# Optimization experiments

Measured on AMD Instinct MI355X. Metric: run time of the kernel, lower is better.

## Reference

```python
import jax, jax.numpy as jnp
import numpy as np
from jax import lax


def setup_inputs() -> dict:
    key = jax.random.key(0)
    ks = jax.random.split(key, 3)
    N, Cin, Cout, H, W = 4, 256, 256, 96, 96
    x = jax.random.normal(ks[0], (N, Cin, H, W), jnp.float32)
    # DCNv2-style internal offset/mask conv: 27 = 9 dy + 9 dx + 9 mask logits
    w_off = jax.random.normal(ks[1], (27, Cin, 3, 3), jnp.float32) * 0.01
    b_off = jnp.zeros((27,), jnp.float32)
    w = jax.random.normal(ks[2], (Cout, Cin, 3, 3), jnp.float32) * (1.0 / np.sqrt(Cin * 9))
    b = jnp.zeros((Cout,), jnp.float32)
    gamma = jnp.ones((Cout,), jnp.float32)
    beta = jnp.zeros((Cout,), jnp.float32)
    return {"x": x, "w_off": w_off, "b_off": b_off, "w": w, "b": b, "gamma": gamma, "beta": beta}


def _bilinear(img, py, px):
    # img: [C,H,W]; py,px: [K,H,W] float sampling coords. Zero outside bounds.
    C, H, W = img.shape
    flat = img.reshape(C, -1)
    y0 = jnp.floor(py)
    x0 = jnp.floor(px)
    ly = py - y0
    lx = px - x0

    def gather(yc, xc):
        valid = (yc >= 0) & (yc <= H - 1) & (xc >= 0) & (xc <= W - 1)
        yi = jnp.clip(yc, 0, H - 1).astype(jnp.int32)
        xi = jnp.clip(xc, 0, W - 1).astype(jnp.int32)
        idx = (yi * W + xi).reshape(-1)
        v = flat[:, idx].reshape((C,) + yc.shape)  # [C,K,H,W]
        return v * valid.astype(img.dtype)

    v00 = gather(y0, x0)
    v01 = gather(y0, x0 + 1)
    v10 = gather(y0 + 1, x0)
    v11 = gather(y0 + 1, x0 + 1)
    return (v00 * (1 - ly) * (1 - lx) + v01 * (1 - ly) * lx
            + v10 * ly * (1 - lx) + v11 * ly * lx)


def _forward(x, w_off, b_off, w, b, gamma, beta):
    N, C, H, W = x.shape
    Cout = w.shape[0]
    dn = ("NCHW", "OIHW", "NCHW")
    # internal offset/mask conv (3x3, stride 1, pad 1)
    om = lax.conv_general_dilated(x, w_off, (1, 1), [(1, 1), (1, 1)], dimension_numbers=dn)
    om = om + b_off[None, :, None, None]
    dy, dx, m = om[:, :9], om[:, 9:18], jax.nn.sigmoid(om[:, 18:])
    # base 3x3 kernel grid, dilation 1, padding 1 (centered taps -1..1)
    ky, kx = jnp.meshgrid(jnp.arange(3) - 1, jnp.arange(3) - 1, indexing="ij")
    py = dy + jnp.arange(H, dtype=x.dtype)[None, None, :, None] + ky.reshape(1, 9, 1, 1).astype(x.dtype)
    px = dx + jnp.arange(W, dtype=x.dtype)[None, None, None, :] + kx.reshape(1, 9, 1, 1).astype(x.dtype)
    sampled = jax.vmap(_bilinear)(x, py, px)  # [N,C,9,H,W]
    sampled = sampled * m[:, None]            # DCNv2 modulation mask
    y = jnp.einsum("nckhw,ock->nohw", sampled, w.reshape(Cout, C, 9))
    y = y + b[None, :, None, None]
    # BatchNorm2d (training-mode batch statistics) + ReLU
    mean = y.mean(axis=(0, 2, 3))
    var = y.var(axis=(0, 2, 3))
    y = (y - mean[None, :, None, None]) * lax.rsqrt(var[None, :, None, None] + 1e-5)
    y = y * gamma[None, :, None, None] + beta[None, :, None, None]
    return jax.nn.relu(y)


def reference(x, w_off, b_off, w, b, gamma, beta):
    return _forward(x, w_off, b_off, w, b, gamma, beta)
```

## Files before the change

### kernel.cpp

```cpp
#include <hip/hip_runtime.h>
#include <cmath>

#define H 96
#define W 96
#define HW 9216
#define CIN 256
#define COUT 256
#define NB 4
#define NCH 72
#define NGR 36

typedef float f32x4 __attribute__((ext_vector_type(4)));
typedef float f32x2 __attribute__((ext_vector_type(2)));
typedef short bf16x8 __attribute__((ext_vector_type(8)));

__device__ __forceinline__ unsigned short f2bf(float f) {
  unsigned int u = __float_as_uint(f);
  u += 0x7fff + ((u >> 16) & 1);
  return (unsigned short)(u >> 16);
}
__device__ __forceinline__ float bf2f(unsigned short u) {
  return __uint_as_float(((unsigned int)u) << 16);
}
__device__ __forceinline__ f32x2 up2(unsigned int u) {
  f32x2 r;
  r.x = __uint_as_float(u << 16);
  r.y = __uint_as_float(u & 0xffff0000u);
  return r;
}
__device__ __forceinline__ unsigned int cvtpk(float lo, float hi) {
  unsigned int r;
  asm("v_cvt_pk_bf16_f32 %0, %1, %2" : "=v"(r) : "v"(lo), "v"(hi));
  return r;
}

__device__ __forceinline__ void bar() {
  asm volatile("s_waitcnt lgkmcnt(0)" ::: "memory");
  __builtin_amdgcn_s_barrier();
  asm volatile("" ::: "memory");
}

__global__ __launch_bounds__(256)
void xt_convert(const float* __restrict__ x, unsigned short* __restrict__ xT) {
  __shared__ unsigned short ls[64][72];
  int tid = threadIdx.x;
  int hwbase = blockIdx.x * 64;
  int cbase  = blockIdx.y * 64;
  int n      = blockIdx.z;

  {
    int cl = tid >> 2, qd = tid & 3;
    const float* src = x + ((size_t)(n * CIN + cbase + cl)) * HW + hwbase + qd * 16;
#pragma unroll
    for (int m = 0; m < 4; ++m) {
      float4 v = *(const float4*)(src + m * 4);
      int hwl = qd * 16 + m * 4;
      ls[hwl + 0][cl] = f2bf(v.x);
      ls[hwl + 1][cl] = f2bf(v.y);
      ls[hwl + 2][cl] = f2bf(v.z);
      ls[hwl + 3][cl] = f2bf(v.w);
    }
  }
  __syncthreads();
  {
    int hw = tid >> 2, part = tid & 3;
    unsigned short* dst = xT + ((size_t)(n * HW + hwbase + hw)) * CIN + cbase + part * 16;
    *(uint4*)(dst + 0) = *(const uint4*)(&ls[hw][part * 16 + 0]);
    *(uint4*)(dst + 8) = *(const uint4*)(&ls[hw][part * 16 + 8]);
  }
}

__global__ __launch_bounds__(256)
void wa_convert(const float* __restrict__ w, unsigned short* __restrict__ Ag) {
  int gid = blockIdx.x * 256 + threadIdx.x;
  int ch = gid >> 10;
  int rest = gid & 1023;
  int ot = rest >> 6, l = rest & 63;
  int o = ot * 16 + (l & 15);
  int k = ch >> 3, cc = ch & 7;
  int cbase = cc * 32 + (l >> 4) * 8;
  unsigned short r[8];
#pragma unroll
  for (int j = 0; j < 8; ++j)
    r[j] = f2bf(w[((size_t)o * CIN + cbase + j) * 9 + k]);
  uint4 pk;
  pk.x = (unsigned int)r[0] | ((unsigned int)r[1] << 16);
  pk.y = (unsigned int)r[2] | ((unsigned int)r[3] << 16);
  pk.z = (unsigned int)r[4] | ((unsigned int)r[5] << 16);
  pk.w = (unsigned int)r[6] | ((unsigned int)r[7] << 16);
  *(uint4*)(Ag + (size_t)gid * 8) = pk;
}

__global__ __launch_bounds__(256)
void wa2_convert(const float* __restrict__ w_off, unsigned short* __restrict__ Ag2) {
  int gid = blockIdx.x * 256 + threadIdx.x;
  int ch = gid >> 7;
  int rest = gid & 127;
  int ot = rest >> 6, l = rest & 63;
  int o = ot * 16 + (l & 15);
  int k = ch >> 3, cc = ch & 7;
  int cbase = cc * 32 + (l >> 4) * 8;
  unsigned short r[8];
#pragma unroll
  for (int j = 0; j < 8; ++j)
    r[j] = (o < 27) ? f2bf(w_off[((size_t)o * CIN + cbase + j) * 9 + k]) : (unsigned short)0;
  uint4 pk;
  pk.x = (unsigned int)r[0] | ((unsigned int)r[1] << 16);
  pk.y = (unsigned int)r[2] | ((unsigned int)r[3] << 16);
  pk.z = (unsigned int)r[4] | ((unsigned int)r[5] << 16);
  pk.w = (unsigned int)r[6] | ((unsigned int)r[7] << 16);
  *(uint4*)(Ag2 + (size_t)gid * 8) = pk;
}

__global__ __launch_bounds__(256, 4)
void offset_gemm(const unsigned short* __restrict__ xT,
                 const unsigned short* __restrict__ Ag2,
                 const float* __restrict__ b_off,
                 float* __restrict__ py, float* __restrict__ px,
                 float* __restrict__ mk) {
  __shared__ int sPos[9][64];
  __shared__ unsigned short sB[2][4096];

  int tid = threadIdx.x;
  int wv = tid >> 6, lane = tid & 63, quad = lane >> 4, l16 = lane & 15;
  int pixBase = blockIdx.x * 64;
  int n = blockIdx.y;
  const unsigned short* xTn = xT + (size_t)n * HW * CIN;

  if (tid < 64) {
    int hwp = pixBase + tid;
    int hh = hwp / W, wx = hwp % W;
#pragma unroll
    for (int ty = 0; ty < 3; ++ty) {
#pragma unroll
      for (int tx = 0; tx < 3; ++tx) {
        int iy = hh + ty - 1, ix = wx + tx - 1;
        bool ok = (iy >= 0) && (iy < H) && (ix >= 0) && (ix < W);
        sPos[ty * 3 + tx][tid] = ok ? (iy * W + ix) : -1;
      }
    }
  }
  bar();

  int pix0 = tid >> 3, ck0 = tid & 7;
  int pix1 = 32 + (tid >> 3);
  int a0 = (ck0 >> 2) * 2048 + (pix0 >> 4) * 512 + ((ck0 & 3) * 16 + ((pix0 & 15) ^ (ck0 & 3))) * 8;
  int a1 = (ck0 >> 2) * 2048 + (pix1 >> 4) * 512 + ((ck0 & 3) * 16 + ((pix1 & 15) ^ (ck0 & 3))) * 8;

  f32x4 acc[2];
  acc[0] = (f32x4){0.f, 0.f, 0.f, 0.f};
  acc[1] = (f32x4){0.f, 0.f, 0.f, 0.f};

  uint4 dA[2], dB[2];
  auto issue = [&](int g, uint4* d) {
    int k = g % 9, c2 = g / 9;
    int p0 = sPos[k][pix0], p1 = sPos[k][pix1];
    d[0] = (uint4){0, 0, 0, 0};
    d[1] = (uint4){0, 0, 0, 0};
    if (p0 >= 0) d[0] = *(const uint4*)(xTn + (size_t)p0 * CIN + c2 * 64 + ck0 * 8);
    if (p1 >= 0) d[1] = *(const uint4*)(xTn + (size_t)p1 * CIN + c2 * 64 + ck0 * 8);
  };

  bf16x8 afr[4];
  auto aload = [&](int g) {
    int k = g % 9, c2 = g / 9;
    int ch = k * 8 + c2 * 2;
#pragma unroll
    for (int s = 0; s < 2; ++s)
#pragma unroll
      for (int ot = 0; ot < 2; ++ot)
        afr[s * 2 + ot] = *(const bf16x8*)(Ag2 + ((size_t)((ch + s) * 2 + ot) * 64 + lane) * 8);
  };

  int rdAddr0 = wv * 512 + (quad * 16 + (l16 ^ quad)) * 8;
  auto mfmaPhase = [&](int buf) {
    __builtin_amdgcn_s_setprio(1);
#pragma unroll
    for (int s = 0; s < 2; ++s) {
      bf16x8 bfr = *(const bf16x8*)(&sB[buf][s * 2048 + rdAddr0]);
      acc[0] = __builtin_amdgcn_mfma_f32_16x16x32_bf16(afr[s * 2 + 0], bfr, acc[0], 0, 0, 0);
      acc[1] = __builtin_amdgcn_mfma_f32_16x16x32_bf16(afr[s * 2 + 1], bfr, acc[1], 0, 0, 0);
    }
    __builtin_amdgcn_s_setprio(0);
  };
  auto store = [&](uint4* d, int buf) {
    *(uint4*)(&sB[buf][a0]) = d[0];
    *(uint4*)(&sB[buf][a1]) = d[1];
  };

  issue(0, dA);
  aload(0);
  store(dA, 0);
  issue(1, dB);
  bar();

  for (int g = 0; g < NGR; g += 2) {
    if (g + 2 < NGR) issue(g + 2, dA);
    mfmaPhase(0);
    aload(g + 1);
    store(dB, 1);
    bar();

    if (g + 3 < NGR) issue(g + 3, dB);
    mfmaPhase(1);
    if (g + 2 < NGR) {
      aload(g + 2);
      store(dA, 0);
      bar();
    }
  }

  int pix = pixBase + wv * 16 + l16;
  int he = pix / W, we = pix % W;
#pragma unroll
  for (int ot = 0; ot < 2; ++ot) {
#pragma unroll
    for (int r = 0; r < 4; ++r) {
      int kk = ot * 16 + quad * 4 + r;
      if (kk >= 27) continue;
      float v = acc[ot][r] + b_off[kk];
      if (kk < 9) {
        py[(size_t)(n * 9 + kk) * HW + pix] = v + (float)he + (float)(kk / 3 - 1);
      } else if (kk < 18) {
        int j = kk - 9;
        px[(size_t)(n * 9 + j) * HW + pix] = v + (float)we + (float)(j % 3 - 1);
      } else {
        mk[(size_t)(n * 9 + (kk - 18)) * HW + pix] = 1.f / (1.f + expf(-v));
      }
    }
  }
}

__global__ __launch_bounds__(512, 4)
void fused_gemm(const unsigned short* __restrict__ xT,
                const unsigned short* __restrict__ Ag,
                const float* __restrict__ py,
                const float* __restrict__ px,
                const float* __restrict__ mk,
                unsigned short* __restrict__ yb,
                float* __restrict__ sumArr, float* __restrict__ sqArr) {
  __shared__ int   sIdx[9][4][64];
  __shared__ float sWgt[9][4][64];
  __shared__ unsigned short sB[2][4096];

  int tid = threadIdx.x;
  int wv = tid >> 6, lane = tid & 63, quad = lane >> 4, l16 = lane & 15;
  int pixBase = blockIdx.x * 64;
  int n = blockIdx.y;
  const unsigned short* xTn = xT + (size_t)n * HW * CIN;

  {
    int pix0 = tid & 63;
    int k0 = tid >> 6;
#pragma unroll
    for (int rep = 0; rep < 2; ++rep) {
      int k = (rep == 0) ? k0 : 8;
      if (rep == 1 && tid >= 64) break;
      int off = (n * 9 + k) * HW + pixBase + pix0;
      float fy = py[off], fx = px[off], fm = mk[off];
      float y0f = floorf(fy), x0f = floorf(fx);
      float ly = fy - y0f, lx = fx - x0f;
      int y0 = (int)y0f, x0 = (int)x0f;
      int cy0 = min(max(y0, 0), H - 1), cy1 = min(max(y0 + 1, 0), H - 1);
      int cx0 = min(max(x0, 0), W - 1), cx1 = min(max(x0 + 1, 0), W - 1);
      float vy0 = (y0 >= 0 && y0 <= H - 1) ? 1.f : 0.f;
      float vy1 = (y0 + 1 >= 0 && y0 + 1 <= H - 1) ? 1.f : 0.f;
      float vx0 = (x0 >= 0 && x0 <= W - 1) ? 1.f : 0.f;
      float vx1 = (x0 + 1 >= 0 && x0 + 1 <= W - 1) ? 1.f : 0.f;
      sIdx[k][0][pix0] = cy0 * W + cx0;
      sIdx[k][1][pix0] = cy0 * W + cx1;
      sIdx[k][2][pix0] = cy1 * W + cx0;
      sIdx[k][3][pix0] = cy1 * W + cx1;
      sWgt[k][0][pix0] = (1.f - ly) * (1.f - lx) * fm * vy0 * vx0;
      sWgt[k][1][pix0] = (1.f - ly) * lx * fm * vy0 * vx1;
      sWgt[k][2][pix0] = ly * (1.f - lx) * fm * vy1 * vx0;
      sWgt[k][3][pix0] = ly * lx * fm * vy1 * vx1;
    }
  }
  bar();

  int pixS  = ((wv & 3) << 4) | (lane >> 2);
  int qS    = lane & 3;
  int chunk = ((wv >> 2) << 2) | qS;
  int co    = chunk * 8;
  int sAddr = (chunk >> 2) * 2048 + (wv & 3) * 512 + (qS * 16 + ((lane >> 2) ^ qS)) * 8;

  f32x4 acc[2][4];
#pragma unroll
  for (int i = 0; i < 2; ++i)
#pragma unroll
    for (int pt = 0; pt < 4; ++pt) acc[i][pt] = (f32x4){0.f, 0.f, 0.f, 0.f};

  uint4 cnA[4], cnB[4];
  float wgA[4], wgB[4];
  auto issue = [&](int g, uint4* cn, float* wt) {
    int k = g % 9, c2 = g / 9;
    int i0 = sIdx[k][0][pixS], i1 = sIdx[k][1][pixS];
    int i2 = sIdx[k][2][pixS], i3 = sIdx[k][3][pixS];
    int coff = c2 * 64 + co;
    cn[0] = *(const uint4*)(xTn + (size_t)i0 * CIN + coff);
    cn[1] = *(const uint4*)(xTn + (size_t)i1 * CIN + coff);
    cn[2] = *(const uint4*)(xTn + (size_t)i2 * CIN + coff);
    cn[3] = *(const uint4*)(xTn + (size_t)i3 * CIN + coff);
    wt[0] = sWgt[k][0][pixS]; wt[1] = sWgt[k][1][pixS];
    wt[2] = sWgt[k][2][pixS]; wt[3] = sWgt[k][3][pixS];
  };

  auto blendOne = [&](unsigned int u0, unsigned int u1, unsigned int u2,
                      unsigned int u3, const float* wt) -> unsigned int {
    f32x2 s = up2(u0) * wt[0];
    s += up2(u1) * wt[1];
    s += up2(u2) * wt[2];
    s += up2(u3) * wt[3];
    return cvtpk(s.x, s.y);
  };
  auto blendStore = [&](uint4* cn, const float* wt, int buf) {
    uint4 r;
    r.x = blendOne(cn[0].x, cn[1].x, cn[2].x, cn[3].x, wt);
    r.y = blendOne(cn[0].y, cn[1].y, cn[2].y, cn[3].y, wt);
    r.z = blendOne(cn[0].z, cn[1].z, cn[2].z, cn[3].z, wt);
    r.w = blendOne(cn[0].w, cn[1].w, cn[2].w, cn[3].w, wt);
    *(uint4*)(&sB[buf][sAddr]) = r;
  };

  bf16x8 afr[4];
  auto aload = [&](int g) {
    int k = g % 9, c2 = g / 9;
    int ch = k * 8 + c2 * 2;
#pragma unroll
    for (int s = 0; s < 2; ++s)
#pragma unroll
      for (int ot = 0; ot < 2; ++ot)
        afr[s * 2 + ot] = *(const bf16x8*)(Ag + ((size_t)((ch + s) * 16 + 2 * wv + ot) * 64 + lane) * 8);
  };

  int rdBase = (quad * 16 + (l16 ^ quad)) * 8;
  auto mfmaPhase = [&](int buf) {
    __builtin_amdgcn_s_setprio(1);
#pragma unroll
    for (int s = 0; s < 2; ++s) {
      bf16x8 bfr[4];
#pragma unroll
      for (int pt = 0; pt < 4; ++pt)
        bfr[pt] = *(const bf16x8*)(&sB[buf][s * 2048 + pt * 512 + rdBase]);
#pragma unroll
      for (int pt = 0; pt < 4; ++pt) {
        acc[0][pt] = __builtin_amdgcn_mfma_f32_16x16x32_bf16(afr[s * 2 + 0], bfr[pt], acc[0][pt], 0, 0, 0);
        acc[1][pt] = __builtin_amdgcn_mfma_f32_16x16x32_bf16(afr[s * 2 + 1], bfr[pt], acc[1][pt], 0, 0, 0);
      }
    }
    __builtin_amdgcn_s_setprio(0);
  };

  issue(0, cnA, wgA);
  aload(0);
  blendStore(cnA, wgA, 0);
  issue(1, cnB, wgB);
  bar();

  for (int g = 0; g < NGR; g += 2) {
    if (g + 2 < NGR) issue(g + 2, cnA, wgA);
    mfmaPhase(0);
    aload(g + 1);
    blendStore(cnB, wgB, 1);
    bar();

    if (g + 3 < NGR) issue(g + 3, cnB, wgB);
    mfmaPhase(1);
    if (g + 2 < NGR) {
      aload(g + 2);
      blendStore(cnA, wgA, 0);
      bar();
    }
  }

#pragma unroll
  for (int ot = 0; ot < 2; ++ot) {
#pragma unroll
    for (int r = 0; r < 4; ++r) {
      int o = (2 * wv + ot) * 16 + quad * 4 + r;
      unsigned short* rowp = yb + (size_t)(n * COUT + o) * HW + pixBase;
      float s = 0.f, q = 0.f;
#pragma unroll
      for (int pt = 0; pt < 4; ++pt) {
        float v = acc[ot][pt][r];
        rowp[pt * 16 + l16] = f2bf(v);
        s += v;
        q = fmaf(v, v, q);
      }
#pragma unroll
      for (int m = 8; m >= 1; m >>= 1) {
        s += __shfl_xor(s, m, 64);
        q += __shfl_xor(q, m, 64);
      }
      if (l16 == 0) {
        atomicAdd(&sumArr[o], s);
        atomicAdd(&sqArr[o], q);
      }
    }
  }
}

__global__ __launch_bounds__(256)
void bn_finalize(const float* __restrict__ sumArr, const float* __restrict__ sqArr,
                 const float* __restrict__ gamma, const float* __restrict__ beta,
                 float* __restrict__ scaleArr, float* __restrict__ shiftArr) {
  int o = threadIdx.x;
  const float inv = 1.f / (float)(NB * HW);
  float mean = sumArr[o] * inv;
  float var = sqArr[o] * inv - mean * mean;
  float sc = rsqrtf(var + 1e-5f) * gamma[o];
  scaleArr[o] = sc;
  shiftArr[o] = beta[o] - mean * sc;
}

__global__ __launch_bounds__(256)
void bn_apply(const unsigned short* __restrict__ yb,
              float* __restrict__ out,
              const float* __restrict__ scaleArr,
              const float* __restrict__ shiftArr) {
  int gid = blockIdx.x * 256 + threadIdx.x;
  int base = gid * 8;
  int o = (base / HW) % COUT;
  float scale = scaleArr[o], shift = shiftArr[o];
  uint4 v = ((const uint4*)yb)[gid];
  float4 a, b;
  a.x = fmaxf(fmaf(bf2f((unsigned short)(v.x & 0xffff)), scale, shift), 0.f);
  a.y = fmaxf(fmaf(bf2f((unsigned short)(v.x >> 16)), scale, shift), 0.f);
  a.z = fmaxf(fmaf(bf2f((unsigned short)(v.y & 0xffff)), scale, shift), 0.f);
  a.w = fmaxf(fmaf(bf2f((unsigned short)(v.y >> 16)), scale, shift), 0.f);
  b.x = fmaxf(fmaf(bf2f((unsigned short)(v.z & 0xffff)), scale, shift), 0.f);
  b.y = fmaxf(fmaf(bf2f((unsigned short)(v.z >> 16)), scale, shift), 0.f);
  b.z = fmaxf(fmaf(bf2f((unsigned short)(v.w & 0xffff)), scale, shift), 0.f);
  b.w = fmaxf(fmaf(bf2f((unsigned short)(v.w >> 16)), scale, shift), 0.f);
  *(float4*)&out[base] = a;
  *(float4*)&out[base + 4] = b;
}

extern "C" void kernel_launch(void* const* d_in, const int* in_sizes, int n_in,
                              void* d_out, int out_size, void* d_ws, size_t ws_size,
                              hipStream_t stream) {
  const float* x     = (const float*)d_in[0];
  const float* w_off = (const float*)d_in[1];
  const float* b_off = (const float*)d_in[2];
  const float* w     = (const float*)d_in[3];
  const float* gamma = (const float*)d_in[5];
  const float* beta  = (const float*)d_in[6];
  float* out = (float*)d_out;

  float* ws = (float*)d_ws;
  float* py = ws;
  float* px = py + 331776;
  float* mk = px + 331776;
  unsigned short* Ag  = (unsigned short*)(mk + 331776);
  unsigned short* Ag2 = Ag + 589824;
  float* sumArr   = (float*)(Ag2 + 73728);
  float* sqArr    = sumArr + 256;
  float* scaleArr = sqArr + 256;
  float* shiftArr = scaleArr + 256;
  unsigned short* yb = (unsigned short*)(shiftArr + 256);
  unsigned short* xT = yb + 9437184;

  hipMemsetAsync(sumArr, 0, 512 * sizeof(float), stream);

  dim3 gT(HW / 64, CIN / 64, NB);
  xt_convert<<<gT, 256, 0, stream>>>(x, xT);

  wa_convert<<<(NCH * 16 * 64) / 256, 256, 0, stream>>>(w, Ag);
  wa2_convert<<<(NCH * 2 * 64) / 256, 256, 0, stream>>>(w_off, Ag2);

  dim3 gO(HW / 64, NB);
  offset_gemm<<<gO, 256, 0, stream>>>(xT, Ag2, b_off, py, px, mk);

  dim3 gG(HW / 64, NB);
  fused_gemm<<<gG, 512, 0, stream>>>(xT, Ag, py, px, mk, yb, sumArr, sqArr);

  bn_finalize<<<1, 256, 0, stream>>>(sumArr, sqArr, gamma, beta, scaleArr, shiftArr);
  bn_apply<<<(NB * COUT * HW / 8) / 256, 256, 0, stream>>>(yb, out, scaleArr, shiftArr);
}
```

Baseline: 279.7 us.

## Halve barriers by staging two K-groups per LDS buffer and vectorize index tables

Both GEMM kernels now keep two K-groups per shared-memory buffer, so each barrier interval covers two MFMA phases instead of one. This halves the number of block-wide syncs and lets the gathers for groups two steps ahead be in flight longer. The fused kernel also stores its bilinear index and weight tables pixel-major, so each lookup is a single 16-byte LDS read instead of eight scalar reads. The cost is double the LDS for sB and a deeper prefetch, which may lower occupancy.

Measured after the change: 258.5 us. -7.6%, faster.

```diff
diff --git a/kernel.cpp b/kernel.cpp
--- a/kernel.cpp
+++ b/kernel.cpp
@@ -9,6 +9,7 @@
 #define NB 4
 #define NCH 72
 #define NGR 36
+#define NIV 18
 
 typedef float f32x4 __attribute__((ext_vector_type(4)));
 typedef float f32x2 __attribute__((ext_vector_type(2)));
@@ -119,7 +120,7 @@
                  float* __restrict__ py, float* __restrict__ px,
                  float* __restrict__ mk) {
   __shared__ int sPos[9][64];
-  __shared__ unsigned short sB[2][4096];
+  __shared__ unsigned short sB[2][2][4096];
 
   int tid = threadIdx.x;
   int wv = tid >> 6, lane = tid & 63, quad = lane >> 4, l16 = lane & 15;
@@ -173,41 +174,42 @@
   };
 
   int rdAddr0 = wv * 512 + (quad * 16 + (l16 ^ quad)) * 8;
-  auto mfmaPhase = [&](int buf) {
+  auto mfmaPhase = [&](int buf, int half) {
+    const unsigned short* base = &sB[buf][half][0];
     __builtin_amdgcn_s_setprio(1);
 #pragma unroll
     for (int s = 0; s < 2; ++s) {
-      bf16x8 bfr = *(const bf16x8*)(&sB[buf][s * 2048 + rdAddr0]);
+      bf16x8 bfr = *(const bf16x8*)(base + s * 2048 + rdAddr0);
       acc[0] = __builtin_amdgcn_mfma_f32_16x16x32_bf16(afr[s * 2 + 0], bfr, acc[0], 0, 0, 0);
       acc[1] = __builtin_amdgcn_mfma_f32_16x16x32_bf16(afr[s * 2 + 1], bfr, acc[1], 0, 0, 0);
     }
     __builtin_amdgcn_s_setprio(0);
   };
-  auto store = [&](uint4* d, int buf) {
-    *(uint4*)(&sB[buf][a0]) = d[0];
-    *(uint4*)(&sB[buf][a1]) = d[1];
+  auto store = [&](uint4* d, int buf, int half) {
+    *(uint4*)(&sB[buf][half][a0]) = d[0];
+    *(uint4*)(&sB[buf][half][a1]) = d[1];
   };
 
   issue(0, dA);
+  issue(1, dB);
   aload(0);
-  store(dA, 0);
-  issue(1, dB);
+  store(dA, 0, 0);
+  issue(2, dA);
+  store(dB, 0, 1);
+  issue(3, dB);
   bar();
 
-  for (int g = 0; g < NGR; g += 2) {
-    if (g + 2 < NGR) issue(g + 2, dA);
-    mfmaPhase(0);
-    aload(g + 1);
-    store(dB, 1);
+  for (int i = 0; i < NIV; ++i) {
+    int buf = i & 1;
+    mfmaPhase(buf, 0);
+    aload(2 * i + 1);
+    if (i < NIV - 1) store(dA, buf ^ 1, 0);
+    if (i < NIV - 2) issue(2 * i + 4, dA);
+    mfmaPhase(buf, 1);
+    if (i < NIV - 1) store(dB, buf ^ 1, 1);
+    if (i < NIV - 2) issue(2 * i + 5, dB);
+    if (i < NIV - 1) aload(2 * i + 2);
     bar();
-
-    if (g + 3 < NGR) issue(g + 3, dB);
-    mfmaPhase(1);
-    if (g + 2 < NGR) {
-      aload(g + 2);
-      store(dA, 0);
-      bar();
-    }
   }
 
   int pix = pixBase + wv * 16 + l16;
@@ -239,9 +241,9 @@
                 const float* __restrict__ mk,
                 unsigned short* __restrict__ yb,
                 float* __restrict__ sumArr, float* __restrict__ sqArr) {
-  __shared__ int   sIdx[9][4][64];
-  __shared__ float sWgt[9][4][64];
-  __shared__ unsigned short sB[2][4096];
+  __shared__ int   sIdx4[9][64][4];
+  __shared__ float sWgt4[9][64][4];
+  __shared__ unsigned short sB[2][2][4096];
 
   int tid = threadIdx.x;
   int wv = tid >> 6, lane = tid & 63, quad = lane >> 4, l16 = lane & 15;
@@ -267,14 +269,18 @@
       float vy1 = (y0 + 1 >= 0 && y0 + 1 <= H - 1) ? 1.f : 0.f;
       float vx0 = (x0 >= 0 && x0 <= W - 1) ? 1.f : 0.f;
       float vx1 = (x0 + 1 >= 0 && x0 + 1 <= W - 1) ? 1.f : 0.f;
-      sIdx[k][0][pix0] = cy0 * W + cx0;
-      sIdx[k][1][pix0] = cy0 * W + cx1;
-      sIdx[k][2][pix0] = cy1 * W + cx0;
-      sIdx[k][3][pix0] = cy1 * W + cx1;
-      sWgt[k][0][pix0] = (1.f - ly) * (1.f - lx) * fm * vy0 * vx0;
-      sWgt[k][1][pix0] = (1.f - ly) * lx * fm * vy0 * vx1;
-      sWgt[k][2][pix0] = ly * (1.f - lx) * fm * vy1 * vx0;
-      sWgt[k][3][pix0] = ly * lx * fm * vy1 * vx1;
+      int4 iv;
+      iv.x = cy0 * W + cx0;
+      iv.y = cy0 * W + cx1;
+      iv.z = cy1 * W + cx0;
+      iv.w = cy1 * W + cx1;
+      float4 wf;
+      wf.x = (1.f - ly) * (1.f - lx) * fm * vy0 * vx0;
+      wf.y = (1.f - ly) * lx * fm * vy0 * vx1;
+      wf.z = ly * (1.f - lx) * fm * vy1 * vx0;
+      wf.w = ly * lx * fm * vy1 * vx1;
+      *(int4*)(&sIdx4[k][pix0][0]) = iv;
+      *(float4*)(&sWgt4[k][pix0][0]) = wf;
     }
   }
   bar();
@@ -295,15 +301,14 @@
   float wgA[4], wgB[4];
   auto issue = [&](int g, uint4* cn, float* wt) {
     int k = g % 9, c2 = g / 9;
-    int i0 = sIdx[k][0][pixS], i1 = sIdx[k][1][pixS];
-    int i2 = sIdx[k][2][pixS], i3 = sIdx[k][3][pixS];
+    int4 iv = *(const int4*)(&sIdx4[k][pixS][0]);
+    float4 wf = *(const float4*)(&sWgt4[k][pixS][0]);
     int coff = c2 * 64 + co;
-    cn[0] = *(const uint4*)(xTn + (size_t)i0 * CIN + coff);
-    cn[1] = *(const uint4*)(xTn + (size_t)i1 * CIN + coff);
-    cn[2] = *(const uint4*)(xTn + (size_t)i2 * CIN + coff);
-    cn[3] = *(const uint4*)(xTn + (size_t)i3 * CIN + coff);
-    wt[0] = sWgt[k][0][pixS]; wt[1] = sWgt[k][1][pixS];
-    wt[2] = sWgt[k][2][pixS]; wt[3] = sWgt[k][3][pixS];
+    cn[0] = *(const uint4*)(xTn + (size_t)iv.x * CIN + coff);
+    cn[1] = *(const uint4*)(xTn + (size_t)iv.y * CIN + coff);
+    cn[2] = *(const uint4*)(xTn + (size_t)iv.z * CIN + coff);
+    cn[3] = *(const uint4*)(xTn + (size_t)iv.w * CIN + coff);
+    wt[0] = wf.x; wt[1] = wf.y; wt[2] = wf.z; wt[3] = wf.w;
   };
 
   auto blendOne = [&](unsigned int u0, unsigned int u1, unsigned int u2,
@@ -314,13 +319,13 @@
     s += up2(u3) * wt[3];
     return cvtpk(s.x, s.y);
   };
-  auto blendStore = [&](uint4* cn, const float* wt, int buf) {
+  auto blendStore = [&](uint4* cn, const float* wt, int buf, int half) {
     uint4 r;
     r.x = blendOne(cn[0].x, cn[1].x, cn[2].x, cn[3].x, wt);
     r.y = blendOne(cn[0].y, cn[1].y, cn[2].y, cn[3].y, wt);
     r.z = blendOne(cn[0].z, cn[1].z, cn[2].z, cn[3].z, wt);
     r.w = blendOne(cn[0].w, cn[1].w, cn[2].w, cn[3].w, wt);
-    *(uint4*)(&sB[buf][sAddr]) = r;
+    *(uint4*)(&sB[buf][half][sAddr]) = r;
   };
 
   bf16x8 afr[4];
@@ -335,14 +340,15 @@
   };
 
   int rdBase = (quad * 16 + (l16 ^ quad)) * 8;
-  auto mfmaPhase = [&](int buf) {
+  auto mfmaPhase = [&](int buf, int half) {
+    const unsigned short* base = &sB[buf][half][0];
     __builtin_amdgcn_s_setprio(1);
 #pragma unroll
     for (int s = 0; s < 2; ++s) {
       bf16x8 bfr[4];
 #pragma unroll
       for (int pt = 0; pt < 4; ++pt)
-        bfr[pt] = *(const bf16x8*)(&sB[buf][s * 2048 + pt * 512 + rdBase]);
+        bfr[pt] = *(const bf16x8*)(base + s * 2048 + pt * 512 + rdBase);
 #pragma unroll
       for (int pt = 0; pt < 4; ++pt) {
         acc[0][pt] = __builtin_amdgcn_mfma_f32_16x16x32_bf16(afr[s * 2 + 0], bfr[pt], acc[0][pt], 0, 0, 0);
@@ -353,25 +359,25 @@
   };
 
   issue(0, cnA, wgA);
+  issue(1, cnB, wgB);
   aload(0);
-  blendStore(cnA, wgA, 0);
-  issue(1, cnB, wgB);
+  blendStore(cnA, wgA, 0, 0);
+  issue(2, cnA, wgA);
+  blendStore(cnB, wgB, 0, 1);
+  issue(3, cnB, wgB);
   bar();
 
-  for (int g = 0; g < NGR; g += 2) {
-    if (g + 2 < NGR) issue(g + 2, cnA, wgA);
-    mfmaPhase(0);
-    aload(g + 1);
-    blendStore(cnB, wgB, 1);
+  for (int i = 0; i < NIV; ++i) {
+    int buf = i & 1;
+    mfmaPhase(buf, 0);
+    aload(2 * i + 1);
+    if (i < NIV - 1) blendStore(cnA, wgA, buf ^ 1, 0);
+    if (i < NIV - 2) issue(2 * i + 4, cnA, wgA);
+    mfmaPhase(buf, 1);
+    if (i < NIV - 1) blendStore(cnB, wgB, buf ^ 1, 1);
+    if (i < NIV - 2) issue(2 * i + 5, cnB, wgB);
+    if (i < NIV - 1) aload(2 * i + 2);
     bar();
-
-    if (g + 3 < NGR) issue(g + 3, cnB, wgB);
-    mfmaPhase(1);
-    if (g + 2 < NGR) {
-      aload(g + 2);
-      blendStore(cnA, wgA, 0);
-      bar();
-    }
   }
 
 #pragma unroll
```
